# Optimization experiments

Hardware: AMD Instinct MI355X
Metric: run time of the kernel (lower is better)

Reference implementation:

```python
import jax, jax.numpy as jnp
import numpy as np

N_NODES = 100000
N_EDGES = 1600000
IN_FEATS = 256
OUT_FEATS = 128


def setup_inputs() -> dict:
    key = jax.random.key(0)
    k1, k2, k3, k4 = jax.random.split(key, 4)
    feat = jax.random.normal(k1, (N_NODES, IN_FEATS), dtype=jnp.float32)
    W = jax.random.normal(k2, (IN_FEATS, OUT_FEATS), dtype=jnp.float32)
    src = jax.random.randint(k3, (N_EDGES,), 0, N_NODES, dtype=jnp.int64)
    dst = jax.random.randint(k4, (N_EDGES,), 0, N_NODES, dtype=jnp.int64)
    return {"feat": feat, "W": W, "src": src, "dst": dst}


def reference(feat, W, src, dst):
    # h_self = feat @ W  -> [N, out_feats]
    h_self = feat @ W
    # update_all(copy_src('h','m'), sum('m','neigh')): gather source features,
    # scatter-sum at destination nodes (SpMM over the edge list).
    msgs = h_self[src]                                        # [E, out_feats]
    h_neigh = jax.ops.segment_sum(msgs, dst, num_segments=N_NODES)
    # in-degree per node
    degs = jax.ops.segment_sum(jnp.ones(dst.shape, jnp.float32), dst,
                               num_segments=N_NODES)          # [N]
    rst = (h_neigh + h_self) / (degs[:, None] + 1.0)
    return jax.nn.relu(rst)
```

## Files before the change

### kernel.cpp

```cpp
#include <hip/hip_runtime.h>
#include <hip/hip_bf16.h>


#define IN_FEATS 256
#define OUT_FEATS 128
#define NUM_NODES 100000
#define NUM_EDGES 1600000

#define NB 782
#define EC 128
#define CHUNK_E 12500
#define BCAP 3072
#define GEMM_BLOCKS 782

typedef __attribute__((ext_vector_type(8))) short short8;
typedef __attribute__((ext_vector_type(8))) unsigned short ushort8;
typedef __attribute__((ext_vector_type(4))) float f32x4;

#define LDA 72

static __device__ inline unsigned short f2bfu(float x) {
    union { __hip_bfloat16 h; unsigned short u; } c;
    c.h = __float2bfloat16(x);
    return c.u;
}
static __device__ inline ushort2 f2bfu2(float x, float y) {
    union { __hip_bfloat162 h; ushort2 u; } c;
    c.h = __float22bfloat162_rn(make_float2(x, y));
    return c.u;
}
static __device__ inline float bf2f(unsigned short h) {
    return __uint_as_float((unsigned)h << 16);
}

__global__ __launch_bounds__(256) void convert_hist(
    const float* __restrict__ W, unsigned short* __restrict__ Wt,
    const int* __restrict__ dst, int* __restrict__ counts)
{
    int b = blockIdx.x;
    int t = threadIdx.x;
    if (b < 128) {
        int i = b * 256 + t;
        int n = i >> 8;
        int k = i & 255;
        Wt[i] = f2bfu(W[(size_t)k * OUT_FEATS + n]);
        return;
    }
    int c = b - 128;
    __shared__ int hist[NB];
    for (int i = t; i < NB; i += 256) hist[i] = 0;
    __syncthreads();
    const int4* dp = (const int4*)(dst + c * CHUNK_E);
    for (int i = t; i < CHUNK_E / 4; i += 256) {
        int4 d4 = dp[i];
        atomicAdd(&hist[d4.x >> 7], 1);
        atomicAdd(&hist[d4.y >> 7], 1);
        atomicAdd(&hist[d4.z >> 7], 1);
        atomicAdd(&hist[d4.w >> 7], 1);
    }
    __syncthreads();
    for (int i = t; i < NB; i += 256) counts[c * NB + i] = hist[i];
}

__global__ __launch_bounds__(128) void scan_chunks(
    int* __restrict__ counts, int* __restrict__ bucket_total)
{
    __shared__ int sd[128];
    int b = blockIdx.x, t = threadIdx.x;
    int v = counts[t * NB + b];
    sd[t] = v;
    __syncthreads();
    for (int o = 1; o < 128; o <<= 1) {
        int x = (t >= o) ? sd[t - o] : 0;
        __syncthreads();
        sd[t] += x;
        __syncthreads();
    }
    counts[t * NB + b] = sd[t] - v;
    if (t == 127) bucket_total[b] = sd[127];
}

__global__ __launch_bounds__(256) void scan_buckets(
    const int* __restrict__ bucket_total, int* __restrict__ bucket_base)
{
    __shared__ int sd[256];
    int t = threadIdx.x;
    int base = t * 4;
    int v0 = 0, v1 = 0, v2 = 0, v3 = 0;
    if (base + 3 < NB) {
        int4 v = *(const int4*)&bucket_total[base];
        v0 = v.x; v1 = v.y; v2 = v.z; v3 = v.w;
    } else {
        if (base + 0 < NB) v0 = bucket_total[base + 0];
        if (base + 1 < NB) v1 = bucket_total[base + 1];
        if (base + 2 < NB) v2 = bucket_total[base + 2];
        if (base + 3 < NB) v3 = bucket_total[base + 3];
    }
    int s = v0 + v1 + v2 + v3;
    sd[t] = s;
    __syncthreads();
    for (int o = 1; o < 256; o <<= 1) {
        int x = (t >= o) ? sd[t - o] : 0;
        __syncthreads();
        sd[t] += x;
        __syncthreads();
    }
    int e0 = sd[t] - s, e1 = e0 + v0, e2 = e1 + v1, e3 = e2 + v2;
    if (base + 0 < NB) bucket_base[base + 0] = e0;
    if (base + 1 < NB) bucket_base[base + 1] = e1;
    if (base + 2 < NB) bucket_base[base + 2] = e2;
    if (base + 3 < NB) bucket_base[base + 3] = e3;
}

__global__ __launch_bounds__(256) void gemm_scatter(
    const float* __restrict__ feat, const unsigned short* __restrict__ Wt,
    unsigned short* __restrict__ hself16, int M,
    const int* __restrict__ src, const int* __restrict__ dst,
    const int* __restrict__ counts, const int* __restrict__ bucket_base,
    int* __restrict__ bedges)
{
    __shared__ char smem_raw[2 * 128 * LDA * 2];

    const int tid = threadIdx.x;

    if (blockIdx.x >= GEMM_BLOCKS) {
        int c = blockIdx.x - GEMM_BLOCKS;
        int* cur = (int*)smem_raw;
        for (int i = tid; i < NB; i += 256)
            cur[i] = bucket_base[i] + counts[c * NB + i];
        __syncthreads();
        const int4* dp = (const int4*)(dst + c * CHUNK_E);
        const int4* sp = (const int4*)(src + c * CHUNK_E);
        for (int i = tid; i < CHUNK_E / 4; i += 256) {
            int4 d4 = dp[i];
            int4 s4 = sp[i];
            int dv[4] = { d4.x, d4.y, d4.z, d4.w };
            int sv[4] = { s4.x, s4.y, s4.z, s4.w };
#pragma unroll
            for (int j = 0; j < 4; ++j) {
                int d = dv[j];
                int slot = atomicAdd(&cur[d >> 7], 1);
                bedges[slot] = sv[j] | ((d & 127) << 17);
            }
        }
        return;
    }

    short* smem  = (short*)smem_raw;
    short* a_lds = smem;
    short* b_lds = smem + 128 * LDA;

    const int w  = tid >> 6;
    const int l  = tid & 63;
    const int lf = l & 15;
    const int lg = l >> 4;
    const int wm = (w & 1) * 64;
    const int wn = (w >> 1) * 64;
    const int bm0 = blockIdx.x * 128;

    f32x4 acc[4][4];
#pragma unroll
    for (int mt = 0; mt < 4; ++mt)
#pragma unroll
        for (int nt = 0; nt < 4; ++nt)
            acc[mt][nt] = (f32x4){0.f, 0.f, 0.f, 0.f};

    const int srow  = tid >> 1;
    const int skseg = (tid & 1) * 32;

    for (int k0 = 0; k0 < IN_FEATS; k0 += 64) {
        int grow = bm0 + srow;
        ushort8* ap = (ushort8*)(a_lds + srow * LDA + skseg);
        if (grow < M) {
            const float4* gp = (const float4*)(feat + (size_t)grow * IN_FEATS + k0 + skseg);
#pragma unroll
            for (int i = 0; i < 4; ++i) {
                float4 v0 = gp[2 * i];
                float4 v1 = gp[2 * i + 1];
                ushort2 c0 = f2bfu2(v0.x, v0.y);
                ushort2 c1 = f2bfu2(v0.z, v0.w);
                ushort2 c2 = f2bfu2(v1.x, v1.y);
                ushort2 c3 = f2bfu2(v1.z, v1.w);
                ushort8 p = { c0.x, c0.y, c1.x, c1.y, c2.x, c2.y, c3.x, c3.y };
                ap[i] = p;
            }
        } else {
            ushort8 z = { 0, 0, 0, 0, 0, 0, 0, 0 };
#pragma unroll
            for (int i = 0; i < 4; ++i) ap[i] = z;
        }
        {
            const ushort8* wp = (const ushort8*)(Wt + (size_t)srow * IN_FEATS + k0 + skseg);
            ushort8* bp = (ushort8*)(b_lds + srow * LDA + skseg);
#pragma unroll
            for (int i = 0; i < 4; ++i) bp[i] = wp[i];
        }
        __syncthreads();

#pragma unroll
        for (int ks = 0; ks < 64; ks += 32) {
            short8 af[4], bfr[4];
#pragma unroll
            for (int mt = 0; mt < 4; ++mt)
                af[mt] = *(const short8*)(a_lds + (wm + mt * 16 + lf) * LDA + ks + lg * 8);
#pragma unroll
            for (int nt = 0; nt < 4; ++nt)
                bfr[nt] = *(const short8*)(b_lds + (wn + nt * 16 + lf) * LDA + ks + lg * 8);
#pragma unroll
            for (int mt = 0; mt < 4; ++mt)
#pragma unroll
                for (int nt = 0; nt < 4; ++nt)
                    acc[mt][nt] = __builtin_amdgcn_mfma_f32_16x16x32_bf16(
                        af[mt], bfr[nt], acc[mt][nt], 0, 0, 0);
        }
        __syncthreads();
    }

    short* ep = smem + w * (64 * LDA);
#pragma unroll
    for (int mt = 0; mt < 4; ++mt)
#pragma unroll
        for (int nt = 0; nt < 4; ++nt)
#pragma unroll
            for (int r = 0; r < 4; r += 2) {
                ushort2 cv = f2bfu2(acc[mt][nt][r], acc[mt][nt][r + 1]);
                ep[(mt * 16 + lg * 4 + r) * LDA + nt * 16 + lf]     = (short)cv.x;
                ep[(mt * 16 + lg * 4 + r + 1) * LDA + nt * 16 + lf] = (short)cv.y;
            }
#pragma unroll
    for (int rr = 0; rr < 8; ++rr) {
        int row = rr * 8 + (l >> 3);
        short8 v = *(const short8*)(ep + row * LDA + (l & 7) * 8);
        int grow = bm0 + wm + row;
        if (grow < M)
            *(short8*)(hself16 + (size_t)grow * OUT_FEATS + wn + (l & 7) * 8) = v;
    }
}

__global__ __launch_bounds__(256) void sort_gather(
    const int* __restrict__ bucket_base, const int* __restrict__ bucket_total,
    const int* __restrict__ bedges, const unsigned short* __restrict__ hself16,
    float* __restrict__ out)
{
    __shared__ int edata[BCAP];
    __shared__ int sorted[BCAP];
    __shared__ int cnt[128], off[128], cursor[128], sd[128];

    int b = blockIdx.x, t = threadIdx.x;
    int base = bucket_base[b];
    int tot = bucket_total[b];
    if (tot > BCAP) tot = BCAP;
    int nnodes = NUM_NODES - b * 128;
    if (nnodes > 128) nnodes = 128;

    if (t < 128) cnt[t] = 0;
    __syncthreads();
    for (int i = t; i < tot; i += 256) {
        int e = bedges[base + i];
        edata[i] = e;
        atomicAdd(&cnt[e >> 17], 1);
    }
    __syncthreads();
    if (t < 128) sd[t] = cnt[t];
    __syncthreads();
    for (int o = 1; o < 128; o <<= 1) {
        int x = 0;
        if (t < 128 && t >= o) x = sd[t - o];
        __syncthreads();
        if (t < 128) sd[t] += x;
        __syncthreads();
    }
    if (t < 128) { int e = sd[t] - cnt[t]; off[t] = e; cursor[t] = e; }
    __syncthreads();
    for (int i = t; i < tot; i += 256) {
        int e = edata[i];
        int r = atomicAdd(&cursor[e >> 17], 1);
        sorted[r] = e & 0x1FFFF;
    }
    __syncthreads();

    int w = t >> 6, l = t & 63, lg = l >> 4, lf = l & 15;
    for (int ln = w; ln < nnodes; ln += 4) {
        int beg = off[ln];
        int end = beg + cnt[ln];
        float acc[8];
#pragma unroll
        for (int i = 0; i < 8; ++i) acc[i] = 0.f;
        for (int j0 = beg; j0 < end; j0 += 8) {
            int ja = j0 + lg;
            int jb = j0 + 4 + lg;
            bool pa = ja < end;
            bool pb = jb < end;
            int sa = pa ? sorted[ja] : 0;
            int sb = pb ? sorted[jb] : 0;
            ushort8 ha = *(const ushort8*)(hself16 + (size_t)sa * OUT_FEATS + lf * 8);
            ushort8 hb = *(const ushort8*)(hself16 + (size_t)sb * OUT_FEATS + lf * 8);
            if (pa) {
#pragma unroll
                for (int i = 0; i < 8; ++i) acc[i] += bf2f(ha[i]);
            }
            if (pb) {
#pragma unroll
                for (int i = 0; i < 8; ++i) acc[i] += bf2f(hb[i]);
            }
        }
#pragma unroll
        for (int i = 0; i < 8; ++i) {
            acc[i] += __shfl_xor(acc[i], 16, 64);
            acc[i] += __shfl_xor(acc[i], 32, 64);
        }
        if (lg == 0) {
            int n = b * 128 + ln;
            float inv = 1.0f / (float)(end - beg + 1);
            ushort8 hs = *(const ushort8*)(hself16 + (size_t)n * OUT_FEATS + lf * 8);
            float v[8];
#pragma unroll
            for (int i = 0; i < 8; ++i)
                v[i] = fmaxf((acc[i] + bf2f(hs[i])) * inv, 0.f);
            float4* op = (float4*)(out + (size_t)n * OUT_FEATS + lf * 8);
            op[0] = make_float4(v[0], v[1], v[2], v[3]);
            op[1] = make_float4(v[4], v[5], v[6], v[7]);
        }
    }
}

extern "C" void kernel_launch(void* const* d_in, const int* in_sizes, int n_in,
                              void* d_out, int out_size, void* d_ws, size_t ws_size,
                              hipStream_t stream) {
    const float* feat = (const float*)d_in[0];
    const float* W    = (const float*)d_in[1];
    const int*   src  = (const int*)d_in[2];
    const int*   dst  = (const int*)d_in[3];
    float* out = (float*)d_out;

    char* ws = (char*)d_ws;
    unsigned short* hself16 = (unsigned short*)ws;
    unsigned short* Wt      = (unsigned short*)(ws + 25600000);
    int* counts       = (int*)(ws + 25665536);
    int* bucket_total = (int*)(ws + 26065920);
    int* bucket_base  = (int*)(ws + 26069120);
    int* bedges       = (int*)(ws + 26072320);

    convert_hist<<<256, 256, 0, stream>>>(W, Wt, dst, counts);

    scan_chunks<<<NB, 128, 0, stream>>>(counts, bucket_total);
    scan_buckets<<<1, 256, 0, stream>>>(bucket_total, bucket_base);

    gemm_scatter<<<GEMM_BLOCKS + EC, 256, 0, stream>>>(
        feat, Wt, hself16, NUM_NODES, src, dst, counts, bucket_base, bedges);

    sort_gather<<<NB, 256, 0, stream>>>(bucket_base, bucket_total, bedges, hself16, out);
}
```

Measured before the change: 304.3 us.

## Keep full W tile resident in swizzled LDS and stream A directly into registers

The GEMM is restructured to use 512-thread blocks covering 256 rows. The whole transposed bf16 weight matrix is loaded once into XOR-swizzled LDS, and each wave loads its feat rows straight from global into MFMA fragments, which removes the per-k-step A staging and the barriers around it. The gather loop in sort_gather now issues four neighbour row loads per iteration instead of two, to raise memory-level parallelism. The 64KB of LDS per block limits occupancy, and the per-lane A loads may coalesce less well than the old cooperative staging.

Result: faster. 289.4 us (-4.9%).

```diff
diff --git a/kernel.cpp b/kernel.cpp
--- a/kernel.cpp
+++ b/kernel.cpp
@@ -11,13 +11,11 @@
 #define EC 128
 #define CHUNK_E 12500
 #define BCAP 3072
-#define GEMM_BLOCKS 782
+#define GEMM_BLOCKS 391
 
 typedef __attribute__((ext_vector_type(8))) short short8;
 typedef __attribute__((ext_vector_type(8))) unsigned short ushort8;
 typedef __attribute__((ext_vector_type(4))) float f32x4;
-
-#define LDA 72
 
 static __device__ inline unsigned short f2bfu(float x) {
     union { __hip_bfloat16 h; unsigned short u; } c;
@@ -112,26 +110,25 @@
     if (base + 3 < NB) bucket_base[base + 3] = e3;
 }
 
-__global__ __launch_bounds__(256) void gemm_scatter(
+__global__ __launch_bounds__(512, 4) void gemm_scatter(
     const float* __restrict__ feat, const unsigned short* __restrict__ Wt,
     unsigned short* __restrict__ hself16, int M,
     const int* __restrict__ src, const int* __restrict__ dst,
     const int* __restrict__ counts, const int* __restrict__ bucket_base,
     int* __restrict__ bedges)
 {
-    __shared__ char smem_raw[2 * 128 * LDA * 2];
-
+    __shared__ char smem_raw[65536];
     const int tid = threadIdx.x;
 
     if (blockIdx.x >= GEMM_BLOCKS) {
         int c = blockIdx.x - GEMM_BLOCKS;
         int* cur = (int*)smem_raw;
-        for (int i = tid; i < NB; i += 256)
+        for (int i = tid; i < NB; i += 512)
             cur[i] = bucket_base[i] + counts[c * NB + i];
         __syncthreads();
         const int4* dp = (const int4*)(dst + c * CHUNK_E);
         const int4* sp = (const int4*)(src + c * CHUNK_E);
-        for (int i = tid; i < CHUNK_E / 4; i += 256) {
+        for (int i = tid; i < CHUNK_E / 4; i += 512) {
             int4 d4 = dp[i];
             int4 s4 = sp[i];
             int dv[4] = { d4.x, d4.y, d4.z, d4.w };
@@ -146,94 +143,93 @@
         return;
     }
 
-    short* smem  = (short*)smem_raw;
-    short* a_lds = smem;
-    short* b_lds = smem + 128 * LDA;
+    unsigned short* Bl = (unsigned short*)smem_raw;
+
+    {
+        int n = tid >> 2;
+        int gbase = (tid & 3) * 8;
+#pragma unroll
+        for (int j = 0; j < 8; ++j) {
+            int g = gbase + j;
+            ushort8 v = *(const ushort8*)(Wt + (size_t)n * IN_FEATS + g * 8);
+            *(ushort8*)(Bl + n * IN_FEATS + ((g ^ (n & 7)) * 8)) = v;
+        }
+    }
+    __syncthreads();
 
     const int w  = tid >> 6;
     const int l  = tid & 63;
     const int lf = l & 15;
-    const int lg = l >> 4;
-    const int wm = (w & 1) * 64;
-    const int wn = (w >> 1) * 64;
-    const int bm0 = blockIdx.x * 128;
-
-    f32x4 acc[4][4];
-#pragma unroll
-    for (int mt = 0; mt < 4; ++mt)
-#pragma unroll
-        for (int nt = 0; nt < 4; ++nt)
+    const int lg = (l >> 4) & 3;
+    const int bm0 = blockIdx.x * 256;
+    const int rbase = bm0 + w * 32;
+
+    f32x4 acc[2][8];
+#pragma unroll
+    for (int mt = 0; mt < 2; ++mt)
+#pragma unroll
+        for (int nt = 0; nt < 8; ++nt)
             acc[mt][nt] = (f32x4){0.f, 0.f, 0.f, 0.f};
 
-    const int srow  = tid >> 1;
-    const int skseg = (tid & 1) * 32;
-
-    for (int k0 = 0; k0 < IN_FEATS; k0 += 64) {
-        int grow = bm0 + srow;
-        ushort8* ap = (ushort8*)(a_lds + srow * LDA + skseg);
-        if (grow < M) {
-            const float4* gp = (const float4*)(feat + (size_t)grow * IN_FEATS + k0 + skseg);
-#pragma unroll
-            for (int i = 0; i < 4; ++i) {
-                float4 v0 = gp[2 * i];
-                float4 v1 = gp[2 * i + 1];
-                ushort2 c0 = f2bfu2(v0.x, v0.y);
-                ushort2 c1 = f2bfu2(v0.z, v0.w);
-                ushort2 c2 = f2bfu2(v1.x, v1.y);
-                ushort2 c3 = f2bfu2(v1.z, v1.w);
-                ushort8 p = { c0.x, c0.y, c1.x, c1.y, c2.x, c2.y, c3.x, c3.y };
-                ap[i] = p;
-            }
-        } else {
-            ushort8 z = { 0, 0, 0, 0, 0, 0, 0, 0 };
-#pragma unroll
-            for (int i = 0; i < 4; ++i) ap[i] = z;
-        }
-        {
-            const ushort8* wp = (const ushort8*)(Wt + (size_t)srow * IN_FEATS + k0 + skseg);
-            ushort8* bp = (ushort8*)(b_lds + srow * LDA + skseg);
-#pragma unroll
-            for (int i = 0; i < 4; ++i) bp[i] = wp[i];
-        }
-        __syncthreads();
-
-#pragma unroll
-        for (int ks = 0; ks < 64; ks += 32) {
-            short8 af[4], bfr[4];
-#pragma unroll
-            for (int mt = 0; mt < 4; ++mt)
-                af[mt] = *(const short8*)(a_lds + (wm + mt * 16 + lf) * LDA + ks + lg * 8);
-#pragma unroll
-            for (int nt = 0; nt < 4; ++nt)
-                bfr[nt] = *(const short8*)(b_lds + (wn + nt * 16 + lf) * LDA + ks + lg * 8);
-#pragma unroll
-            for (int mt = 0; mt < 4; ++mt)
-#pragma unroll
-                for (int nt = 0; nt < 4; ++nt)
-                    acc[mt][nt] = __builtin_amdgcn_mfma_f32_16x16x32_bf16(
-                        af[mt], bfr[nt], acc[mt][nt], 0, 0, 0);
-        }
-        __syncthreads();
-    }
-
-    short* ep = smem + w * (64 * LDA);
-#pragma unroll
-    for (int mt = 0; mt < 4; ++mt)
-#pragma unroll
-        for (int nt = 0; nt < 4; ++nt)
-#pragma unroll
-            for (int r = 0; r < 4; r += 2) {
-                ushort2 cv = f2bfu2(acc[mt][nt][r], acc[mt][nt][r + 1]);
-                ep[(mt * 16 + lg * 4 + r) * LDA + nt * 16 + lf]     = (short)cv.x;
-                ep[(mt * 16 + lg * 4 + r + 1) * LDA + nt * 16 + lf] = (short)cv.y;
-            }
-#pragma unroll
-    for (int rr = 0; rr < 8; ++rr) {
-        int row = rr * 8 + (l >> 3);
-        short8 v = *(const short8*)(ep + row * LDA + (l & 7) * 8);
-        int grow = bm0 + wm + row;
+#pragma unroll 2
+    for (int k0 = 0; k0 < IN_FEATS; k0 += 32) {
+        int k8 = k0 >> 3;
+        short8 af[2];
+#pragma unroll
+        for (int mt = 0; mt < 2; ++mt) {
+            int grow = rbase + mt * 16 + lf;
+            if (grow < M) {
+                const float4* ap = (const float4*)(feat + (size_t)grow * IN_FEATS + k0 + lg * 8);
+                float4 f0 = ap[0];
+                float4 f1 = ap[1];
+                ushort2 c0 = f2bfu2(f0.x, f0.y);
+                ushort2 c1 = f2bfu2(f0.z, f0.w);
+                ushort2 c2 = f2bfu2(f1.x, f1.y);
+                ushort2 c3 = f2bfu2(f1.z, f1.w);
+                af[mt] = (short8){ (short)c0.x, (short)c0.y, (short)c1.x, (short)c1.y,
+                                   (short)c2.x, (short)c2.y, (short)c3.x, (short)c3.y };
+            } else {
+                af[mt] = (short8){ 0, 0, 0, 0, 0, 0, 0, 0 };
+            }
+        }
+#pragma unroll
+        for (int nh = 0; nh < 2; ++nh) {
+            short8 bf[4];
+#pragma unroll
+            for (int q = 0; q < 4; ++q) {
+                int nt = nh * 4 + q;
+                int n = nt * 16 + lf;
+                int g = (k8 + lg) ^ (lf & 7);
+                bf[q] = *(const short8*)(Bl + n * IN_FEATS + g * 8);
+            }
+#pragma unroll
+            for (int q = 0; q < 4; ++q) {
+                int nt = nh * 4 + q;
+                acc[0][nt] = __builtin_amdgcn_mfma_f32_16x16x32_bf16(af[0], bf[q], acc[0][nt], 0, 0, 0);
+                acc[1][nt] = __builtin_amdgcn_mfma_f32_16x16x32_bf16(af[1], bf[q], acc[1][nt], 0, 0, 0);
+            }
+        }
+    }
+
+    __syncthreads();
+    unsigned short* ep = (unsigned short*)smem_raw;
+#pragma unroll
+    for (int mt = 0; mt < 2; ++mt)
+#pragma unroll
+        for (int nt = 0; nt < 8; ++nt)
+#pragma unroll
+            for (int r = 0; r < 4; ++r) {
+                int row = w * 32 + mt * 16 + lg * 4 + r;
+                ep[row * 128 + nt * 16 + lf] = f2bfu(acc[mt][nt][r]);
+            }
+    __syncthreads();
+#pragma unroll
+    for (int i = 0; i < 8; ++i) {
+        int lrow = w * 32 + i * 4 + (l >> 4);
+        ushort8 v = *(const ushort8*)(ep + lrow * 128 + (l & 15) * 8);
+        int grow = bm0 + lrow;
         if (grow < M)
-            *(short8*)(hself16 + (size_t)grow * OUT_FEATS + wn + (l & 7) * 8) = v;
+            *(ushort8*)(hself16 + (size_t)grow * OUT_FEATS + (l & 15) * 8) = v;
     }
 }
 
@@ -286,23 +282,26 @@
         float acc[8];
 #pragma unroll
         for (int i = 0; i < 8; ++i) acc[i] = 0.f;
-        for (int j0 = beg; j0 < end; j0 += 8) {
-            int ja = j0 + lg;
-            int jb = j0 + 4 + lg;
-            bool pa = ja < end;
-            bool pb = jb < end;
-            int sa = pa ? sorted[ja] : 0;
-            int sb = pb ? sorted[jb] : 0;
-            ushort8 ha = *(const ushort8*)(hself16 + (size_t)sa * OUT_FEATS + lf * 8);
-            ushort8 hb = *(const ushort8*)(hself16 + (size_t)sb * OUT_FEATS + lf * 8);
-            if (pa) {
-#pragma unroll
-                for (int i = 0; i < 8; ++i) acc[i] += bf2f(ha[i]);
-            }
-            if (pb) {
-#pragma unroll
-                for (int i = 0; i < 8; ++i) acc[i] += bf2f(hb[i]);
-            }
+        for (int j0 = beg; j0 < end; j0 += 16) {
+            int  jj[4];
+            bool pp[4];
+            int  ss[4];
+#pragma unroll
+            for (int q = 0; q < 4; ++q) {
+                jj[q] = j0 + q * 4 + lg;
+                pp[q] = jj[q] < end;
+                ss[q] = pp[q] ? sorted[jj[q]] : 0;
+            }
+            ushort8 h[4];
+#pragma unroll
+            for (int q = 0; q < 4; ++q)
+                h[q] = *(const ushort8*)(hself16 + (size_t)ss[q] * OUT_FEATS + lf * 8);
+#pragma unroll
+            for (int q = 0; q < 4; ++q)
+                if (pp[q]) {
+#pragma unroll
+                    for (int i = 0; i < 8; ++i) acc[i] += bf2f(h[q][i]);
+                }
         }
 #pragma unroll
         for (int i = 0; i < 8; ++i) {
@@ -342,12 +341,9 @@
     int* bedges       = (int*)(ws + 26072320);
 
     convert_hist<<<256, 256, 0, stream>>>(W, Wt, dst, counts);
-
     scan_chunks<<<NB, 128, 0, stream>>>(counts, bucket_total);
     scan_buckets<<<1, 256, 0, stream>>>(bucket_total, bucket_base);
-
-    gemm_scatter<<<GEMM_BLOCKS + EC, 256, 0, stream>>>(
+    gemm_scatter<<<GEMM_BLOCKS + EC, 512, 0, stream>>>(
         feat, Wt, hself16, NUM_NODES, src, dst, counts, bucket_base, bedges);
-
     sort_gather<<<NB, 256, 0, stream>>>(bucket_base, bucket_total, bedges, hself16, out);
 }
```
